# Kernel optimization log

Measured on AMD Instinct MI355X. Metric: run time of the kernel, lower is better.

Reference implementation:

```python
import jax, jax.numpy as jnp
import numpy as np

BATCH, N_FEATURES, D_MODEL = 8192, 8192, 1024


def setup_inputs() -> dict:
    key = jax.random.key(0)
    kx, kw = jax.random.split(key)
    # x: sparse feature activations in the original (COO); dense uniform here.
    x = jax.random.uniform(kx, (BATCH, N_FEATURES), dtype=jnp.float32)
    # Xavier-normal init for W_tr [n_features, d_model].
    std = float(np.sqrt(2.0 / (N_FEATURES + D_MODEL)))
    W_tr = jax.random.normal(kw, (N_FEATURES, D_MODEL), dtype=jnp.float32) * std
    bias = jnp.zeros((N_FEATURES,), dtype=jnp.float32)
    return {"x": x, "W_tr": W_tr, "bias": bias}


def reference(x, W_tr, bias):
    # h = x @ W_tr              : [B, n_features] @ [n_features, d_model] -> [B, d_model]
    # out = relu(h @ W_tr.T + b): [B, d_model] @ [d_model, n_features] -> [B, n_features]
    h = jnp.einsum("bf,fd->bd", x, W_tr)
    return jax.nn.relu(jnp.einsum("bd,fd->bf", h, W_tr) + bias)
```

## Files before the change

kernel.cpp:

```cpp
#include <hip/hip_runtime.h>
#include <hip/hip_bf16.h>
#include <stdint.h>

#define BATCH  8192
#define NFEAT  8192
#define DMODEL 1024

typedef unsigned short u16;
typedef __attribute__((ext_vector_type(8))) short  short8;
typedef __attribute__((ext_vector_type(4))) float  f32x4;

__device__ __forceinline__ u16 f2b(float f) {
    uint32_t u = __float_as_uint(f);
    u += 0x7fffu + ((u >> 16) & 1u);
    return (u16)(u >> 16);
}

__device__ __forceinline__ void gld16(const u16* g, void* l) {
    __builtin_amdgcn_global_load_lds(
        (const __attribute__((address_space(1))) void*)(uintptr_t)g,
        (__attribute__((address_space(3))) void*)(uint32_t)(uintptr_t)l,
        16, 0, 0);
}


__global__ void cvt_x_kernel(const float* __restrict__ x, u16* __restrict__ xb) {
    int i = blockIdx.x * blockDim.x + threadIdx.x;
    const float4* xv = (const float4*)x;
    float4 a = xv[2 * i];
    float4 b = xv[2 * i + 1];
    union { u16 u[8]; uint4 v; } o;
    o.u[0] = f2b(a.x); o.u[1] = f2b(a.y); o.u[2] = f2b(a.z); o.u[3] = f2b(a.w);
    o.u[4] = f2b(b.x); o.u[5] = f2b(b.y); o.u[6] = f2b(b.z); o.u[7] = f2b(b.w);
    ((uint4*)xb)[i] = o.v;
}

__global__ void cvt_w_kernel(const float* __restrict__ W,
                             u16* __restrict__ wb, u16* __restrict__ wt) {
    __shared__ u16 tile[64][65];
    const int f0 = blockIdx.x * 64;
    const int d0 = blockIdx.y * 64;
    const int t  = threadIdx.x;
#pragma unroll
    for (int rep = 0; rep < 16; ++rep) {
        int idx = rep * 256 + t;
        int r = idx >> 6, c = idx & 63;
        float v = W[(size_t)(f0 + r) * DMODEL + d0 + c];
        u16 u = f2b(v);
        tile[r][c] = u;
        wb[(size_t)(f0 + r) * DMODEL + d0 + c] = u;
    }
    __syncthreads();
#pragma unroll
    for (int rep = 0; rep < 16; ++rep) {
        int idx = rep * 256 + t;
        int r = idx >> 6, c = idx & 63;
        wt[(size_t)(d0 + r) * NFEAT + f0 + c] = tile[c][r];
    }
}

#define CBAR() do { asm volatile("" ::: "memory"); __builtin_amdgcn_s_barrier(); } while (0)


__global__ __launch_bounds__(512, 2)
void gemm1_pipe(const u16* __restrict__ A, const u16* __restrict__ B,
                u16* __restrict__ H, int N, int K) {
    const int NT = K >> 6;
    __shared__ __align__(1024) char lds[131072];
    const int BOFF = 98304;

    const int tid  = threadIdx.x;
    const int lane = tid & 63;
    const int wave = tid >> 6;
    const int wm   = wave >> 2;
    const int wn   = wave & 3;

    const int nwg = gridDim.x;
    const int swz = (blockIdx.x & 7) * (nwg >> 3) + (blockIdx.x >> 3);
    const int ntn = N >> 7;
    const int tm0 = (swz / ntn) << 8;
    const int tn0 = (swz % ntn) << 7;

    const int sr8 = lane >> 3;
    const int sg  = (lane & 7) ^ sr8;
    const int l15 = lane & 15, lhi = lane >> 4;
    const int ch0 = ((lhi ^ (lane & 7)) << 4);

    auto STAGE_A = [&](int tau) {
        if (tau < NT) {
            char* d = lds + (tau % 3) * 32768 + wave * 4096;
#pragma unroll
            for (int i = 0; i < 4; ++i)
                gld16(A + (size_t)(tm0 + wave * 32 + i * 8 + sr8) * K + ((size_t)tau << 6) + sg * 8,
                      d + i * 1024);
        }
    };
    auto STAGE_B = [&](int tau) {
        if (tau < NT) {
            char* d = lds + BOFF + (tau & 1) * 16384 + wave * 2048;
#pragma unroll
            for (int i = 0; i < 2; ++i)
                gld16(B + (size_t)(tn0 + wave * 16 + i * 8 + sr8) * K + ((size_t)tau << 6) + sg * 8,
                      d + i * 1024);
        }
    };

    short8 a0X[4][2], a0Y[4][2], a1[4][2];
    short8 bX[2][2], bY[2][2];
    f32x4  acc[8][2] = {};

#define PREF(T, A0P, BP) do {                                                   \
        if ((T) < NT) {                                                         \
            const char* Abp = lds + ((T) % 3) * 32768 + wm * 16384 + l15 * 128; \
            const char* Bbp = lds + BOFF + ((T) & 1) * 16384 + wn * 4096 + l15 * 128; \
            _Pragma("unroll")                                                   \
            for (int fm = 0; fm < 4; ++fm) {                                    \
                A0P[fm][0] = *(const short8*)(Abp + fm * 2048 + ch0);           \
                A0P[fm][1] = *(const short8*)(Abp + fm * 2048 + (ch0 ^ 64));    \
            }                                                                   \
            _Pragma("unroll")                                                   \
            for (int nh = 0; nh < 2; ++nh) {                                    \
                BP[nh][0] = *(const short8*)(Bbp + nh * 2048 + ch0);            \
                BP[nh][1] = *(const short8*)(Bbp + nh * 2048 + (ch0 ^ 64));     \
            }                                                                   \
        }                                                                       \
    } while (0)

#define MMA0_(A0C, BC) do {                                                     \
        _Pragma("unroll")                                                       \
        for (int nh = 0; nh < 2; ++nh)                                          \
            _Pragma("unroll")                                                   \
            for (int ks = 0; ks < 2; ++ks)                                      \
                _Pragma("unroll")                                               \
                for (int fm = 0; fm < 4; ++fm)                                  \
                    acc[fm][nh] = __builtin_amdgcn_mfma_f32_16x16x32_bf16(      \
                        A0C[fm][ks], BC[nh][ks], acc[fm][nh], 0, 0, 0);         \
    } while (0)

#define MMA1_(BC) do {                                                          \
        _Pragma("unroll")                                                       \
        for (int nh = 0; nh < 2; ++nh)                                          \
            _Pragma("unroll")                                                   \
            for (int ks = 0; ks < 2; ++ks)                                      \
                _Pragma("unroll")                                               \
                for (int fm = 0; fm < 4; ++fm)                                  \
                    acc[4 + fm][nh] = __builtin_amdgcn_mfma_f32_16x16x32_bf16(  \
                        a1[fm][ks], BC[nh][ks], acc[4 + fm][nh], 0, 0, 0);      \
    } while (0)

#define GTILE(T, A0C, BC, A0P, BP) do {                                         \
                  \
        const char* Ab_ = lds + ((T) % 3) * 32768 + wm * 16384 + l15 * 128;     \
        _Pragma("unroll")                                                       \
        for (int fm = 0; fm < 4; ++fm) {                                        \
            a1[fm][0] = *(const short8*)(Ab_ + (4 + fm) * 2048 + ch0);          \
            a1[fm][1] = *(const short8*)(Ab_ + (4 + fm) * 2048 + (ch0 ^ 64));   \
        }                                                                       \
        STAGE_A((T) + 2);                                                       \
        __builtin_amdgcn_s_setprio(1);                                          \
        MMA0_(A0C, BC);                                                         \
        __builtin_amdgcn_s_setprio(0);                                          \
        STAGE_B((T) + 2);                                                       \
                    \
        if ((T) < NT - 2) asm volatile("s_waitcnt vmcnt(6)" ::: "memory");      \
        else              asm volatile("s_waitcnt vmcnt(0)" ::: "memory");      \
        CBAR();             \
        PREF((T) + 1, A0P, BP);                                                 \
        __builtin_amdgcn_s_setprio(1);                                          \
        MMA1_(BC);                                                              \
        __builtin_amdgcn_s_setprio(0);                                          \
    } while (0)

    STAGE_A(0); STAGE_B(0);
    STAGE_A(1); STAGE_B(1);
    asm volatile("s_waitcnt vmcnt(6)" ::: "memory");
    __builtin_amdgcn_s_barrier();
    PREF(0, a0X, bX);

    for (int t = 0; t < NT; t += 2) {
        GTILE(t,     a0X, bX, a0Y, bY);
        GTILE(t + 1, a0Y, bY, a0X, bX);
    }
    __syncthreads();

    u16* lu = (u16*)lds;
#pragma unroll
    for (int fm = 0; fm < 8; ++fm)
#pragma unroll
        for (int nh = 0; nh < 2; ++nh) {
            const int col  = wn * 32 + nh * 16 + l15;
            const int row0 = wm * 128 + fm * 16 + lhi * 4;
#pragma unroll
            for (int r = 0; r < 4; ++r)
                lu[(row0 + r) * 128 + col] = f2b(acc[fm][nh][r]);
        }
    __syncthreads();
    const uint4* ls = (const uint4*)lds;
#pragma unroll
    for (int s = 0; s < 8; ++s) {
        int i = s * 512 + tid;
        int row = i >> 4;
        int col = (i & 15) * 8;
        *(uint4*)(H + (size_t)(tm0 + row) * N + (tn0 + col)) = ls[i];
    }
#undef GTILE
#undef PREF
#undef MMA0_
#undef MMA1_
}

__global__ __launch_bounds__(512, 2)
void gemm2_persist(const u16* __restrict__ A, const u16* __restrict__ B,
                   float* __restrict__ O, const float* __restrict__ bias,
                   int N, int K) {
    __shared__ __align__(1024) char lds[163840];
    const int BOFF = 98304;
    const int TTOT = 64;

    const int tid  = threadIdx.x;
    const int lane = tid & 63;
    const int wave = tid >> 6;
    const int wm   = wave >> 2;
    const int wn   = wave & 3;

    const int bid = blockIdx.x;
    const int xcd = bid & 7;
    const int sub = (bid >> 3) & 3;
    const int mg  = bid >> 5;
    const int tn0     = ((xcd << 2) + sub) << 8;
    const int tm_base = mg << 10;

    const int sr8 = lane >> 3;
    const int sg  = (lane & 7) ^ sr8;
    const int l15 = lane & 15, lhi = lane >> 4;
    const int ch0 = ((lhi ^ (lane & 7)) << 4);

    auto STAGE_A = [&](int tau) {
        if (tau < TTOT) {
            char* d = lds + (tau % 3) * 32768 + wave * 4096;
            const int rb = tm_base + ((tau >> 4) << 8) + wave * 32 + sr8;
            const size_t co = ((size_t)(tau & 15) << 6) + sg * 8;
#pragma unroll
            for (int i = 0; i < 4; ++i)
                gld16(A + (size_t)(rb + i * 8) * K + co, d + i * 1024);
        }
    };
    auto STAGE_B = [&](int tau) {
        if (tau < TTOT) {
            char* d = lds + BOFF + (tau & 1) * 32768 + wave * 4096;
            const int rb = tn0 + wave * 32 + sr8;
            const size_t co = ((size_t)(tau & 15) << 6) + sg * 8;
#pragma unroll
            for (int i = 0; i < 4; ++i)
                gld16(B + (size_t)(rb + i * 8) * K + co, d + i * 1024);
        }
    };

    short8 a0[4][2], a1[4][2];
    short8 b[4][2];
    f32x4  acc[8][4] = {};

    const char* Ab;
    const char* Bb;
    auto LDA0 = [&] {
#pragma unroll
        for (int fm = 0; fm < 4; ++fm) {
            a0[fm][0] = *(const short8*)(Ab + fm * 2048 + ch0);
            a0[fm][1] = *(const short8*)(Ab + fm * 2048 + (ch0 ^ 64));
        }
    };
    auto LDA1 = [&] {
#pragma unroll
        for (int fm = 0; fm < 4; ++fm) {
            a1[fm][0] = *(const short8*)(Ab + (4 + fm) * 2048 + ch0);
            a1[fm][1] = *(const short8*)(Ab + (4 + fm) * 2048 + (ch0 ^ 64));
        }
    };
    auto LDB_ = [&](int nh) {
#pragma unroll
        for (int fn = 0; fn < 2; ++fn) {
            b[nh * 2 + fn][0] = *(const short8*)(Bb + (nh * 2 + fn) * 2048 + ch0);
            b[nh * 2 + fn][1] = *(const short8*)(Bb + (nh * 2 + fn) * 2048 + (ch0 ^ 64));
        }
    };
    auto MMA0 = [&](int nh) {
#pragma unroll
        for (int ks = 0; ks < 2; ++ks)
#pragma unroll
            for (int fm = 0; fm < 4; ++fm)
#pragma unroll
                for (int fn = 0; fn < 2; ++fn)
                    acc[fm][nh * 2 + fn] = __builtin_amdgcn_mfma_f32_16x16x32_bf16(
                        a0[fm][ks], b[nh * 2 + fn][ks], acc[fm][nh * 2 + fn], 0, 0, 0);
    };
    auto MMA1 = [&](int nh) {
#pragma unroll
        for (int ks = 0; ks < 2; ++ks)
#pragma unroll
            for (int fm = 0; fm < 4; ++fm)
#pragma unroll
                for (int fn = 0; fn < 2; ++fn)
                    acc[4 + fm][nh * 2 + fn] = __builtin_amdgcn_mfma_f32_16x16x32_bf16(
                        a1[fm][ks], b[nh * 2 + fn][ks], acc[4 + fm][nh * 2 + fn], 0, 0, 0);
    };

    const int ocol = tn0 + wn * 64;
    float bv[4];
#pragma unroll
    for (int fn = 0; fn < 4; ++fn) bv[fn] = bias[ocol + fn * 16 + l15];

    STAGE_A(0); STAGE_B(0);
    STAGE_A(1); STAGE_B(1);
    asm volatile("s_waitcnt vmcnt(8)" ::: "memory");
    __builtin_amdgcn_s_barrier();

    for (int tt = 0; tt < TTOT; ++tt) {
        Ab = lds + (tt % 3) * 32768 + wm * 16384 + l15 * 128;
        Bb = lds + BOFF + (tt & 1) * 32768 + wn * 8192 + l15 * 128;

        LDB_(0); LDB_(1); LDA0(); LDA1();
        STAGE_A(tt + 2);
        __builtin_amdgcn_s_setprio(1);
        MMA0(0); MMA0(1);
        __builtin_amdgcn_s_setprio(0);
        CBAR();
        STAGE_B(tt + 2);
        __builtin_amdgcn_s_setprio(1);
        MMA1(1); MMA1(0);
        __builtin_amdgcn_s_setprio(0);
        if (tt < TTOT - 2)       asm volatile("s_waitcnt vmcnt(8)" ::: "memory");
        else if (tt == TTOT - 2) asm volatile("s_waitcnt vmcnt(0)" ::: "memory");
        CBAR();

        if ((tt & 15) == 15) {
            const int orow = tm_base + ((tt >> 4) << 8) + wm * 128;
#pragma unroll
            for (int fm = 0; fm < 8; ++fm) {
                const int row0 = orow + fm * 16 + lhi * 4;
#pragma unroll
                for (int fn = 0; fn < 4; ++fn) {
                    const int col = ocol + fn * 16 + l15;
#pragma unroll
                    for (int r = 0; r < 4; ++r) {
                        float v = acc[fm][fn][r] + bv[fn];
                        O[(size_t)(row0 + r) * N + col] = v > 0.f ? v : 0.f;
                        acc[fm][fn][r] = 0.f;
                    }
                }
            }
        }
    }
}


extern "C" void kernel_launch(void* const* d_in, const int* in_sizes, int n_in,
                              void* d_out, int out_size, void* d_ws, size_t ws_size,
                              hipStream_t stream) {
    const float* x    = (const float*)d_in[0];
    const float* W    = (const float*)d_in[1];
    const float* bias = (const float*)d_in[2];
    float* out = (float*)d_out;

    char* ws = (char*)d_ws;
    u16* xb = (u16*)ws;
    u16* wt = (u16*)(ws + 134217728);
    u16* wb = (u16*)(ws + 134217728 + 16777216);
    u16* hb = (u16*)(ws + 134217728 + 2 * 16777216);

    cvt_x_kernel<<<(BATCH * NFEAT / 8) / 256, 256, 0, stream>>>(x, xb);
    cvt_w_kernel<<<dim3(NFEAT / 64, DMODEL / 64), 256, 0, stream>>>(W, wb, wt);

    gemm1_pipe<<<dim3((BATCH / 256) * (DMODEL / 128)), 512, 0, stream>>>(
        xb, wt, hb, DMODEL, NFEAT);

    gemm2_persist<<<dim3(256), 512, 0, stream>>>(
        hb, wb, out, bias, NFEAT, DMODEL);
}
```

Before: 345.7 us.

## Rebuild gemm2 on gemm1's register-prefetch pipeline with 256x128 tiles

```diff
diff --git a/kernel.cpp b/kernel.cpp
--- a/kernel.cpp
+++ b/kernel.cpp
@@ -61,53 +61,6 @@
 
 #define CBAR() do { asm volatile("" ::: "memory"); __builtin_amdgcn_s_barrier(); } while (0)
 
-
-__global__ __launch_bounds__(512, 2)
-void gemm1_pipe(const u16* __restrict__ A, const u16* __restrict__ B,
-                u16* __restrict__ H, int N, int K) {
-    const int NT = K >> 6;
-    __shared__ __align__(1024) char lds[131072];
-    const int BOFF = 98304;
-
-    const int tid  = threadIdx.x;
-    const int lane = tid & 63;
-    const int wave = tid >> 6;
-    const int wm   = wave >> 2;
-    const int wn   = wave & 3;
-
-    const int nwg = gridDim.x;
-    const int swz = (blockIdx.x & 7) * (nwg >> 3) + (blockIdx.x >> 3);
-    const int ntn = N >> 7;
-    const int tm0 = (swz / ntn) << 8;
-    const int tn0 = (swz % ntn) << 7;
-
-    const int sr8 = lane >> 3;
-    const int sg  = (lane & 7) ^ sr8;
-    const int l15 = lane & 15, lhi = lane >> 4;
-    const int ch0 = ((lhi ^ (lane & 7)) << 4);
-
-    auto STAGE_A = [&](int tau) {
-        if (tau < NT) {
-            char* d = lds + (tau % 3) * 32768 + wave * 4096;
-#pragma unroll
-            for (int i = 0; i < 4; ++i)
-                gld16(A + (size_t)(tm0 + wave * 32 + i * 8 + sr8) * K + ((size_t)tau << 6) + sg * 8,
-                      d + i * 1024);
-        }
-    };
-    auto STAGE_B = [&](int tau) {
-        if (tau < NT) {
-            char* d = lds + BOFF + (tau & 1) * 16384 + wave * 2048;
-#pragma unroll
-            for (int i = 0; i < 2; ++i)
-                gld16(B + (size_t)(tn0 + wave * 16 + i * 8 + sr8) * K + ((size_t)tau << 6) + sg * 8,
-                      d + i * 1024);
-        }
-    };
-
-    short8 a0X[4][2], a0Y[4][2], a1[4][2];
-    short8 bX[2][2], bY[2][2];
-    f32x4  acc[8][2] = {};
 
 #define PREF(T, A0P, BP) do {                                                   \
         if ((T) < NT) {                                                         \
@@ -149,7 +102,6 @@
     } while (0)
 
 #define GTILE(T, A0C, BC, A0P, BP) do {                                         \
-                  \
         const char* Ab_ = lds + ((T) % 3) * 32768 + wm * 16384 + l15 * 128;     \
         _Pragma("unroll")                                                       \
         for (int fm = 0; fm < 4; ++fm) {                                        \
@@ -161,7 +113,6 @@
         MMA0_(A0C, BC);                                                         \
         __builtin_amdgcn_s_setprio(0);                                          \
         STAGE_B((T) + 2);                                                       \
-                    \
         if ((T) < NT - 2) asm volatile("s_waitcnt vmcnt(6)" ::: "memory");      \
         else              asm volatile("s_waitcnt vmcnt(0)" ::: "memory");      \
         CBAR();             \
@@ -171,6 +122,53 @@
         __builtin_amdgcn_s_setprio(0);                                          \
     } while (0)
 
+__global__ __launch_bounds__(512, 2)
+void gemm1_pipe(const u16* __restrict__ A, const u16* __restrict__ B,
+                u16* __restrict__ H, int N, int K) {
+    const int NT = K >> 6;
+    __shared__ __align__(1024) char lds[131072];
+    const int BOFF = 98304;
+
+    const int tid  = threadIdx.x;
+    const int lane = tid & 63;
+    const int wave = tid >> 6;
+    const int wm   = wave >> 2;
+    const int wn   = wave & 3;
+
+    const int nwg = gridDim.x;
+    const int swz = (blockIdx.x & 7) * (nwg >> 3) + (blockIdx.x >> 3);
+    const int ntn = N >> 7;
+    const int tm0 = (swz / ntn) << 8;
+    const int tn0 = (swz % ntn) << 7;
+
+    const int sr8 = lane >> 3;
+    const int sg  = (lane & 7) ^ sr8;
+    const int l15 = lane & 15, lhi = lane >> 4;
+    const int ch0 = ((lhi ^ (lane & 7)) << 4);
+
+    auto STAGE_A = [&](int tau) {
+        if (tau < NT) {
+            char* d = lds + (tau % 3) * 32768 + wave * 4096;
+#pragma unroll
+            for (int i = 0; i < 4; ++i)
+                gld16(A + (size_t)(tm0 + wave * 32 + i * 8 + sr8) * K + ((size_t)tau << 6) + sg * 8,
+                      d + i * 1024);
+        }
+    };
+    auto STAGE_B = [&](int tau) {
+        if (tau < NT) {
+            char* d = lds + BOFF + (tau & 1) * 16384 + wave * 2048;
+#pragma unroll
+            for (int i = 0; i < 2; ++i)
+                gld16(B + (size_t)(tn0 + wave * 16 + i * 8 + sr8) * K + ((size_t)tau << 6) + sg * 8,
+                      d + i * 1024);
+        }
+    };
+
+    short8 a0X[4][2], a0Y[4][2], a1[4][2];
+    short8 bX[2][2], bY[2][2];
+    f32x4  acc[8][2] = {};
+
     STAGE_A(0); STAGE_B(0);
     STAGE_A(1); STAGE_B(1);
     asm volatile("s_waitcnt vmcnt(6)" ::: "memory");
@@ -203,19 +201,15 @@
         int col = (i & 15) * 8;
         *(uint4*)(H + (size_t)(tm0 + row) * N + (tn0 + col)) = ls[i];
     }
-#undef GTILE
-#undef PREF
-#undef MMA0_
-#undef MMA1_
 }
 
 __global__ __launch_bounds__(512, 2)
-void gemm2_persist(const u16* __restrict__ A, const u16* __restrict__ B,
-                   float* __restrict__ O, const float* __restrict__ bias,
-                   int N, int K) {
-    __shared__ __align__(1024) char lds[163840];
+void gemm2_pipe(const u16* __restrict__ A, const u16* __restrict__ B,
+                float* __restrict__ O, const float* __restrict__ bias,
+                int N, int K) {
+    const int NT = 128;
+    __shared__ __align__(1024) char lds[131072];
     const int BOFF = 98304;
-    const int TTOT = 64;
 
     const int tid  = threadIdx.x;
     const int lane = tid & 63;
@@ -224,11 +218,10 @@
     const int wn   = wave & 3;
 
     const int bid = blockIdx.x;
-    const int xcd = bid & 7;
-    const int sub = (bid >> 3) & 3;
-    const int mg  = bid >> 5;
-    const int tn0     = ((xcd << 2) + sub) << 8;
-    const int tm_base = mg << 10;
+    const int cp  = ((bid & 7) << 3) | ((bid >> 3) & 7);
+    const int mg  = bid >> 6;
+    const int tn0     = cp << 7;
+    const int tm_base = mg << 11;
 
     const int sr8 = lane >> 3;
     const int sg  = (lane & 7) ^ sr8;
@@ -236,7 +229,7 @@
     const int ch0 = ((lhi ^ (lane & 7)) << 4);
 
     auto STAGE_A = [&](int tau) {
-        if (tau < TTOT) {
+        if (tau < NT) {
             char* d = lds + (tau % 3) * 32768 + wave * 4096;
             const int rb = tm_base + ((tau >> 4) << 8) + wave * 32 + sr8;
             const size_t co = ((size_t)(tau & 15) << 6) + sg * 8;
@@ -246,111 +239,59 @@
         }
     };
     auto STAGE_B = [&](int tau) {
-        if (tau < TTOT) {
-            char* d = lds + BOFF + (tau & 1) * 32768 + wave * 4096;
-            const int rb = tn0 + wave * 32 + sr8;
+        if (tau < NT) {
+            char* d = lds + BOFF + (tau & 1) * 16384 + wave * 2048;
             const size_t co = ((size_t)(tau & 15) << 6) + sg * 8;
 #pragma unroll
-            for (int i = 0; i < 4; ++i)
-                gld16(B + (size_t)(rb + i * 8) * K + co, d + i * 1024);
+            for (int i = 0; i < 2; ++i)
+                gld16(B + (size_t)(tn0 + wave * 16 + i * 8 + sr8) * K + co, d + i * 1024);
         }
     };
 
-    short8 a0[4][2], a1[4][2];
-    short8 b[4][2];
-    f32x4  acc[8][4] = {};
-
-    const char* Ab;
-    const char* Bb;
-    auto LDA0 = [&] {
-#pragma unroll
-        for (int fm = 0; fm < 4; ++fm) {
-            a0[fm][0] = *(const short8*)(Ab + fm * 2048 + ch0);
-            a0[fm][1] = *(const short8*)(Ab + fm * 2048 + (ch0 ^ 64));
-        }
-    };
-    auto LDA1 = [&] {
-#pragma unroll
-        for (int fm = 0; fm < 4; ++fm) {
-            a1[fm][0] = *(const short8*)(Ab + (4 + fm) * 2048 + ch0);
-            a1[fm][1] = *(const short8*)(Ab + (4 + fm) * 2048 + (ch0 ^ 64));
-        }
-    };
-    auto LDB_ = [&](int nh) {
-#pragma unroll
-        for (int fn = 0; fn < 2; ++fn) {
-            b[nh * 2 + fn][0] = *(const short8*)(Bb + (nh * 2 + fn) * 2048 + ch0);
-            b[nh * 2 + fn][1] = *(const short8*)(Bb + (nh * 2 + fn) * 2048 + (ch0 ^ 64));
-        }
-    };
-    auto MMA0 = [&](int nh) {
-#pragma unroll
-        for (int ks = 0; ks < 2; ++ks)
-#pragma unroll
-            for (int fm = 0; fm < 4; ++fm)
-#pragma unroll
-                for (int fn = 0; fn < 2; ++fn)
-                    acc[fm][nh * 2 + fn] = __builtin_amdgcn_mfma_f32_16x16x32_bf16(
-                        a0[fm][ks], b[nh * 2 + fn][ks], acc[fm][nh * 2 + fn], 0, 0, 0);
-    };
-    auto MMA1 = [&](int nh) {
-#pragma unroll
-        for (int ks = 0; ks < 2; ++ks)
-#pragma unroll
-            for (int fm = 0; fm < 4; ++fm)
-#pragma unroll
-                for (int fn = 0; fn < 2; ++fn)
-                    acc[4 + fm][nh * 2 + fn] = __builtin_amdgcn_mfma_f32_16x16x32_bf16(
-                        a1[fm][ks], b[nh * 2 + fn][ks], acc[4 + fm][nh * 2 + fn], 0, 0, 0);
-    };
-
-    const int ocol = tn0 + wn * 64;
-    float bv[4];
-#pragma unroll
-    for (int fn = 0; fn < 4; ++fn) bv[fn] = bias[ocol + fn * 16 + l15];
+    short8 a0X[4][2], a0Y[4][2], a1[4][2];
+    short8 bX[2][2], bY[2][2];
+    f32x4  acc[8][2] = {};
+
+    const int ocol = tn0 + wn * 32;
+    float bv[2];
+#pragma unroll
+    for (int nh = 0; nh < 2; ++nh) bv[nh] = bias[ocol + nh * 16 + l15];
 
     STAGE_A(0); STAGE_B(0);
     STAGE_A(1); STAGE_B(1);
-    asm volatile("s_waitcnt vmcnt(8)" ::: "memory");
+    asm volatile("s_waitcnt vmcnt(6)" ::: "memory");
     __builtin_amdgcn_s_barrier();
-
-    for (int tt = 0; tt < TTOT; ++tt) {
-        Ab = lds + (tt % 3) * 32768 + wm * 16384 + l15 * 128;
-        Bb = lds + BOFF + (tt & 1) * 32768 + wn * 8192 + l15 * 128;
-
-        LDB_(0); LDB_(1); LDA0(); LDA1();
-        STAGE_A(tt + 2);
-        __builtin_amdgcn_s_setprio(1);
-        MMA0(0); MMA0(1);
-        __builtin_amdgcn_s_setprio(0);
-        CBAR();
-        STAGE_B(tt + 2);
-        __builtin_amdgcn_s_setprio(1);
-        MMA1(1); MMA1(0);
-        __builtin_amdgcn_s_setprio(0);
-        if (tt < TTOT - 2)       asm volatile("s_waitcnt vmcnt(8)" ::: "memory");
-        else if (tt == TTOT - 2) asm volatile("s_waitcnt vmcnt(0)" ::: "memory");
-        CBAR();
-
-        if ((tt & 15) == 15) {
-            const int orow = tm_base + ((tt >> 4) << 8) + wm * 128;
+    PREF(0, a0X, bX);
+
+    for (int t = 0; t < NT; t += 2) {
+        GTILE(t,     a0X, bX, a0Y, bY);
+        GTILE(t + 1, a0Y, bY, a0X, bX);
+
+        if (((t + 1) & 15) == 15) {
+            const int seg  = (t + 1) >> 4;
+            const int orow = tm_base + (seg << 8) + wm * 128;
 #pragma unroll
             for (int fm = 0; fm < 8; ++fm) {
                 const int row0 = orow + fm * 16 + lhi * 4;
 #pragma unroll
-                for (int fn = 0; fn < 4; ++fn) {
-                    const int col = ocol + fn * 16 + l15;
+                for (int nh = 0; nh < 2; ++nh) {
+                    const int col = ocol + nh * 16 + l15;
 #pragma unroll
                     for (int r = 0; r < 4; ++r) {
-                        float v = acc[fm][fn][r] + bv[fn];
+                        float v = acc[fm][nh][r] + bv[nh];
                         O[(size_t)(row0 + r) * N + col] = v > 0.f ? v : 0.f;
-                        acc[fm][fn][r] = 0.f;
+                        acc[fm][nh][r] = 0.f;
                     }
                 }
             }
         }
     }
 }
+
+#undef GTILE
+#undef PREF
+#undef MMA0_
+#undef MMA1_
 
 
 extern "C" void kernel_launch(void* const* d_in, const int* in_sizes, int n_in,
@@ -373,6 +314,6 @@
     gemm1_pipe<<<dim3((BATCH / 256) * (DMODEL / 128)), 512, 0, stream>>>(
         xb, wt, hb, DMODEL, NFEAT);
 
-    gemm2_persist<<<dim3(256), 512, 0, stream>>>(
+    gemm2_pipe<<<dim3(256), 512, 0, stream>>>(
         hb, wb, out, bias, NFEAT, DMODEL);
 }
```

After: 352.6 us. Within noise of the previous version (+2.0%).
